# Kernel optimization log

Hardware: AMD Instinct MI355X
Metric: run time of the kernel (lower is better)

Reference implementation:

```python
import jax, jax.numpy as jnp
import numpy as np

NEG_PENALTY = 0.03
B, C_TOTAL, C_LOADED = 2048, 1000, 256


def setup_inputs() -> dict:
    key = jax.random.key(0)
    k1, k2, k3 = jax.random.split(key, 3)
    ranks = jax.random.normal(k1, (B, C_TOTAL), dtype=jnp.float32)
    labels = jax.random.randint(k2, (B, C_TOTAL), 0, 2, dtype=jnp.int32)
    class_ids_loaded = jnp.sort(jax.random.randint(k3, (C_LOADED,), 0, C_TOTAL, dtype=jnp.int64))
    return {"ranks": ranks, "labels": labels, "class_ids_loaded": class_ids_loaded}


def reference(ranks, labels, class_ids_loaded):
    # Select loaded classes: [B, C]
    lab = labels[:, class_ids_loaded].astype(ranks.dtype)
    r = ranks[:, class_ids_loaded]
    pos = lab            # 1 where label == 1 (correct)
    neg = 1.0 - lab      # 1 where label == 0 (wrong)
    # Pairwise hinge: relu(penalty + wrong_rank - correct_rank) over all (correct p, wrong n) pairs.
    # pen[b, p, n] = relu(NEG_PENALTY + r[b, n] - r[b, p]); mask after relu == computing only valid pairs.
    pen = jax.nn.relu(NEG_PENALTY + r[:, None, :] - r[:, :, None])  # [B, C, C]
    total = jnp.einsum('bpn,bp,bn->', pen, pos, neg)
    # Denominator: number of rows with at least one positive label.
    n_valid = jnp.sum(jnp.any(lab == 1.0, axis=1)).astype(ranks.dtype)
    return (total / n_valid).reshape((1,))
```

## Files before the change

kernel.cpp:

```cpp
#include <hip/hip_runtime.h>

#define B_ROWS 2048
#define C_TOTAL 1000
#define C_LOADED 256
#define NEG_PEN 0.03f
#define WPB 4
#define GRID (B_ROWS / WPB)
#define TAG 0x5A5A0000u


union PVU { unsigned long long u; float2 f; };

template<int QMAX>
__device__ __forceinline__ float pair_loop(const float4* __restrict__ n4, int G,
                                           float rp0, float rp1,
                                           float rp2, float rp3) {
    float a0 = 0.f, a1 = 0.f, a2 = 0.f, a3 = 0.f;
    for (int g = 0; g < G; g += 2) {
        float4 x = n4[g];
        float4 y = n4[g + 1];
        float v[8] = {x.x, x.y, x.z, x.w, y.x, y.y, y.z, y.w};
#pragma unroll
        for (int e = 0; e < 8; ++e) {
            a0 += fmaxf(v[e] - rp0, 0.f);
            if (QMAX > 1) a1 += fmaxf(v[e] - rp1, 0.f);
            if (QMAX > 2) a2 += fmaxf(v[e] - rp2, 0.f);
            if (QMAX > 3) a3 += fmaxf(v[e] - rp3, 0.f);
        }
    }
    return (a0 + a1) + (a2 + a3);
}

__global__ void __launch_bounds__(256)
rank_loss_fused(const float* __restrict__ ranks,
                const int* __restrict__ labels,
                const int* __restrict__ ids,
                unsigned long long* __restrict__ pv,
                float* __restrict__ out) {
    __shared__ __align__(16) float negl[WPB][264];
    __shared__ __align__(16) float posl[WPB][256];

    const int t = threadIdx.x;
    const int lane = t & 63;
    const int wave = t >> 6;
    const int row = blockIdx.x * WPB + wave;

    const int c0 = ids[lane];
    const int c1 = ids[lane + 64];
    const int c2 = ids[lane + 128];
    const int c3 = ids[lane + 192];
    const int base = row * C_TOTAL;
    const float r0 = ranks[base + c0], r1 = ranks[base + c1];
    const float r2 = ranks[base + c2], r3 = ranks[base + c3];
    const int l0 = labels[base + c0], l1 = labels[base + c1];
    const int l2 = labels[base + c2], l3 = labels[base + c3];

    const unsigned long long m0 = __ballot(l0 == 0);
    const unsigned long long m1 = __ballot(l1 == 0);
    const unsigned long long m2 = __ballot(l2 == 0);
    const unsigned long long m3 = __ballot(l3 == 0);
    const int n0 = __popcll(m0), n1 = __popcll(m1);
    const int n2 = __popcll(m2), n3 = __popcll(m3);
    const int N = n0 + n1 + n2 + n3;
    const int P = C_LOADED - N;
    const unsigned long long lm = (1ULL << lane) - 1ULL;

    float* ng = negl[wave];
    float* ps = posl[wave];
    const int nb1 = n0, nb2 = n0 + n1, nb3 = n0 + n1 + n2;
    const int pb1 = 64 - n0, pb2 = 128 - nb2, pb3 = 192 - nb3;
    if (l0 == 0) ng[__popcll(m0 & lm)] = r0 + NEG_PEN;
    else         ps[__popcll(~m0 & lm)] = r0;
    if (l1 == 0) ng[nb1 + __popcll(m1 & lm)] = r1 + NEG_PEN;
    else         ps[pb1 + __popcll(~m1 & lm)] = r1;
    if (l2 == 0) ng[nb2 + __popcll(m2 & lm)] = r2 + NEG_PEN;
    else         ps[pb2 + __popcll(~m2 & lm)] = r2;
    if (l3 == 0) ng[nb3 + __popcll(m3 & lm)] = r3 + NEG_PEN;
    else         ps[pb3 + __popcll(~m3 & lm)] = r3;

    const int Npad = (N + 7) & ~7;
    if (lane < Npad - N) ng[N + lane] = -1e30f;

    asm volatile("s_waitcnt lgkmcnt(0)" ::: "memory");

    float acc = 0.f;
    if (P > 0) {
        const int qmax = (P + 63) >> 6;
        float rp0 = 3e30f, rp1 = 3e30f, rp2 = 3e30f, rp3 = 3e30f;
        if (lane < P)       rp0 = ps[lane];
        if (lane + 64 < P)  rp1 = ps[lane + 64];
        if (lane + 128 < P) rp2 = ps[lane + 128];
        if (lane + 192 < P) rp3 = ps[lane + 192];
        const float4* n4 = (const float4*)ng;
        const int G = Npad >> 2;
        switch (qmax) {
        case 1:  acc = pair_loop<1>(n4, G, rp0, rp1, rp2, rp3); break;
        case 2:  acc = pair_loop<2>(n4, G, rp0, rp1, rp2, rp3); break;
        case 3:  acc = pair_loop<3>(n4, G, rp0, rp1, rp2, rp3); break;
        default: acc = pair_loop<4>(n4, G, rp0, rp1, rp2, rp3); break;
        }
    }

#pragma unroll
    for (int off = 32; off > 0; off >>= 1) {
        acc += __shfl_down(acc, off, 64);
    }

    if (lane == 0) {
        PVU v;
        v.f.x = acc;
        v.u = (v.u & 0xFFFFFFFFull) |
              ((unsigned long long)(TAG | ((P > 0) ? 1u : 0u)) << 32);
        (void)__hip_atomic_exchange(&pv[row], v.u, __ATOMIC_RELAXED,
                                    __HIP_MEMORY_SCOPE_AGENT);
    }

    if (row == B_ROWS - 1) {
        float ss = 0.f, sv = 0.f;
#pragma unroll
        for (int grp = 0; grp < 4; ++grp) {
            unsigned long long u[8];
            bool ok;
            do {
#pragma unroll
                for (int k = 0; k < 8; ++k) {
                    u[k] = __hip_atomic_load(
                        &pv[(grp * 8 + k) * 64 + lane],
                        __ATOMIC_RELAXED, __HIP_MEMORY_SCOPE_AGENT);
                }
                unsigned int okm = 1u;
#pragma unroll
                for (int k = 0; k < 8; ++k) {
                    okm &= (((unsigned int)(u[k] >> 32) & 0xFFFFFFFEu) == TAG);
                }
                ok = __all(okm);
            } while (!ok);
#pragma unroll
            for (int k = 0; k < 8; ++k) {
                PVU v; v.u = u[k];
                ss += v.f.x;
                sv += (float)((unsigned int)(u[k] >> 32) & 1u);
            }
        }
#pragma unroll
        for (int off = 32; off > 0; off >>= 1) {
            ss += __shfl_down(ss, off, 64);
            sv += __shfl_down(sv, off, 64);
        }
        if (lane == 0) out[0] = ss / sv;
    }
}

extern "C" void kernel_launch(void* const* d_in, const int* in_sizes, int n_in,
                              void* d_out, int out_size, void* d_ws, size_t ws_size,
                              hipStream_t stream) {
    const float* ranks  = (const float*)d_in[0];
    const int*   labels = (const int*)d_in[1];
    const int*   ids    = (const int*)d_in[2];
    float* out = (float*)d_out;

    unsigned long long* pv = (unsigned long long*)d_ws;

    rank_loss_fused<<<GRID, 256, 0, stream>>>(ranks, labels, ids, pv, out);
}
```

Before: 12.63 us.

## Split each row's positive set across two waves per row

Each block now handles two rows, with two waves per row instead of one. Each wave takes the interleaved half of the positives, so a lane holds at most two positive ranks instead of four. Both waves still rebuild the same compacted negative and positive lists redundantly, and their partial sums are combined through shared memory after a block barrier. This doubles the grid and shortens each wave's serial pair loop, at the cost of duplicated gather and compaction work plus a __syncthreads.

```diff
diff --git a/kernel.cpp b/kernel.cpp
--- a/kernel.cpp
+++ b/kernel.cpp
@@ -4,8 +4,8 @@
 #define C_TOTAL 1000
 #define C_LOADED 256
 #define NEG_PEN 0.03f
-#define WPB 4
-#define GRID (B_ROWS / WPB)
+#define RPB 2
+#define GRID (B_ROWS / RPB)
 #define TAG 0x5A5A0000u
 
 
@@ -13,9 +13,8 @@
 
 template<int QMAX>
 __device__ __forceinline__ float pair_loop(const float4* __restrict__ n4, int G,
-                                           float rp0, float rp1,
-                                           float rp2, float rp3) {
-    float a0 = 0.f, a1 = 0.f, a2 = 0.f, a3 = 0.f;
+                                           float rp0, float rp1) {
+    float a0 = 0.f, a1 = 0.f;
     for (int g = 0; g < G; g += 2) {
         float4 x = n4[g];
         float4 y = n4[g + 1];
@@ -24,11 +23,9 @@
         for (int e = 0; e < 8; ++e) {
             a0 += fmaxf(v[e] - rp0, 0.f);
             if (QMAX > 1) a1 += fmaxf(v[e] - rp1, 0.f);
-            if (QMAX > 2) a2 += fmaxf(v[e] - rp2, 0.f);
-            if (QMAX > 3) a3 += fmaxf(v[e] - rp3, 0.f);
         }
     }
-    return (a0 + a1) + (a2 + a3);
+    return a0 + a1;
 }
 
 __global__ void __launch_bounds__(256)
@@ -37,13 +34,15 @@
                 const int* __restrict__ ids,
                 unsigned long long* __restrict__ pv,
                 float* __restrict__ out) {
-    __shared__ __align__(16) float negl[WPB][264];
-    __shared__ __align__(16) float posl[WPB][256];
+    __shared__ __align__(16) float negl[4][264];
+    __shared__ __align__(16) float posl[4][256];
+    __shared__ float wave_sums[4];
 
     const int t = threadIdx.x;
     const int lane = t & 63;
     const int wave = t >> 6;
-    const int row = blockIdx.x * WPB + wave;
+    const int row = blockIdx.x * RPB + (wave >> 1);
+    const int half = wave & 1;
 
     const int c0 = ids[lane];
     const int c1 = ids[lane + 64];
@@ -83,39 +82,36 @@
 
     asm volatile("s_waitcnt lgkmcnt(0)" ::: "memory");
 
+    const int Ph = (P + 1 - half) >> 1;
     float acc = 0.f;
-    if (P > 0) {
-        const int qmax = (P + 63) >> 6;
-        float rp0 = 3e30f, rp1 = 3e30f, rp2 = 3e30f, rp3 = 3e30f;
-        if (lane < P)       rp0 = ps[lane];
-        if (lane + 64 < P)  rp1 = ps[lane + 64];
-        if (lane + 128 < P) rp2 = ps[lane + 128];
-        if (lane + 192 < P) rp3 = ps[lane + 192];
+    if (Ph > 0) {
+        const int s0 = 2 * lane + half;
+        const int s1 = s0 + 128;
+        const float rp0 = (s0 < P) ? ps[s0] : 3e30f;
+        const float rp1 = (s1 < P) ? ps[s1] : 3e30f;
         const float4* n4 = (const float4*)ng;
         const int G = Npad >> 2;
-        switch (qmax) {
-        case 1:  acc = pair_loop<1>(n4, G, rp0, rp1, rp2, rp3); break;
-        case 2:  acc = pair_loop<2>(n4, G, rp0, rp1, rp2, rp3); break;
-        case 3:  acc = pair_loop<3>(n4, G, rp0, rp1, rp2, rp3); break;
-        default: acc = pair_loop<4>(n4, G, rp0, rp1, rp2, rp3); break;
-        }
+        if (Ph > 64) acc = pair_loop<2>(n4, G, rp0, rp1);
+        else         acc = pair_loop<1>(n4, G, rp0, rp1);
     }
 
 #pragma unroll
     for (int off = 32; off > 0; off >>= 1) {
         acc += __shfl_down(acc, off, 64);
     }
+    if (lane == 0) wave_sums[wave] = acc;
+    __syncthreads();
 
-    if (lane == 0) {
+    if (half == 0 && lane == 0) {
         PVU v;
-        v.f.x = acc;
+        v.f.x = wave_sums[wave] + wave_sums[wave + 1];
         v.u = (v.u & 0xFFFFFFFFull) |
               ((unsigned long long)(TAG | ((P > 0) ? 1u : 0u)) << 32);
         (void)__hip_atomic_exchange(&pv[row], v.u, __ATOMIC_RELAXED,
                                     __HIP_MEMORY_SCOPE_AGENT);
     }
 
-    if (row == B_ROWS - 1) {
+    if (row == B_ROWS - 1 && half == 0) {
         float ss = 0.f, sv = 0.f;
 #pragma unroll
         for (int grp = 0; grp < 4; ++grp) {
```

New measurement: 13.18 us. 4.4% more time.
